# Performance work log

Measured on AMD Instinct MI355X. Metric: run time of the kernel, lower is better.

## Reference

```python
import jax, jax.numpy as jnp
import numpy as np

SEQ = 4096
E = 2048

def setup_inputs() -> dict:
    key = jax.random.key(0)
    kx, kq, kk, kv = jax.random.split(key, 4)
    scale = 1.0 / np.sqrt(E)
    x = jax.random.normal(kx, (SEQ, E), dtype=jnp.float32)
    # nn.Linear weights: shape [out, in], applied as x @ W.T
    Wq = jax.random.uniform(kq, (E, E), dtype=jnp.float32, minval=-scale, maxval=scale)
    Wk = jax.random.uniform(kk, (E, E), dtype=jnp.float32, minval=-scale, maxval=scale)
    Wv = jax.random.uniform(kv, (E, E), dtype=jnp.float32, minval=-scale, maxval=scale)
    return {"x": x, "Wq": Wq, "Wk": Wk, "Wv": Wv}

def reference(x, Wq, Wk, Wv):
    # q/k/v projections: nn.Linear(bias=False) -> x @ W.T
    q = x @ Wq.T  # [S, E]
    k = x @ Wk.T  # [S, E]
    v = x @ Wv.T  # [S, E]
    s = q @ k.T  # [S, S]
    w = jax.nn.softmax(s / jnp.sqrt(jnp.float32(E)), axis=-1)
    return w @ v  # [S, E]
```

## Files before the change

kernel.cpp:

```cpp
#include <hip/hip_runtime.h>
#include <hip/hip_bf16.h>

#define S_DIM 4096
#define E_DIM 2048

typedef __attribute__((ext_vector_type(4))) float f32x4;
typedef __attribute__((ext_vector_type(8))) short bf16x8;

__device__ __forceinline__ unsigned short f2bf(float f) {
  unsigned u = __builtin_bit_cast(unsigned, f);
  u += 0x7FFFu + ((u >> 16) & 1u);
  return (unsigned short)(u >> 16);
}
__device__ __forceinline__ float bf2f(unsigned short h) {
  return __builtin_bit_cast(float, ((unsigned)h) << 16);
}

__global__ __launch_bounds__(256) void cast_kernel(const float* __restrict__ in,
                                                   unsigned short* __restrict__ out,
                                                   int n4) {
  int i = blockIdx.x * 256 + threadIdx.x;
  if (i >= n4) return;
  float4 v = reinterpret_cast<const float4*>(in)[i];
  ushort4 o;
  o.x = f2bf(v.x); o.y = f2bf(v.y); o.z = f2bf(v.z); o.w = f2bf(v.w);
  reinterpret_cast<ushort4*>(out)[i] = o;
}

__global__ __launch_bounds__(256) void cast3_kernel(const float* __restrict__ w0,
                                                    const float* __restrict__ w1,
                                                    const float* __restrict__ w2,
                                                    unsigned short* __restrict__ out,
                                                    int n4each) {
  int i = blockIdx.x * 256 + threadIdx.x;
  if (i >= 3 * n4each) return;
  const float* src = (i < n4each) ? w0 : (i < 2 * n4each ? w1 : w2);
  int j = (i < n4each) ? i : (i < 2 * n4each ? i - n4each : i - 2 * n4each);
  float4 v = reinterpret_cast<const float4*>(src)[j];
  ushort4 o;
  o.x = f2bf(v.x); o.y = f2bf(v.y); o.z = f2bf(v.z); o.w = f2bf(v.w);
  reinterpret_cast<ushort4*>(out)[i] = o;
}

__device__ __forceinline__ void stage_half128(const unsigned short* __restrict__ g,
                                              int grow0, int ld, int kByte0,
                                              char* base, int tid) {
#pragma unroll
  for (int p = 0; p < 4; ++p) {
    const int o = (p * 256 + tid) * 16;
    const int S = o >> 10;
    const int oi = o & 1023;
    const int osi = oi ^ (((oi >> 9) & 1) << 5);
    const int r  = (S >> 1) * 16 + (osi >> 6);
    const int cb = (S & 1) * 64 + (osi & 63);
    const char* ga = reinterpret_cast<const char*>(g) +
                     ((size_t)(grow0 + r) * ld) * 2 + kByte0 + cb;
    char* la = base + (o & ~1023);
    __builtin_amdgcn_global_load_lds(
        (const __attribute__((address_space(1))) void*)ga,
        (__attribute__((address_space(3))) void*)la, 16, 0, 0);
  }
}


enum { EPI_QKV = 0, EPI_BF16 = 1, EPI_F32 = 2 };

template <int EPI>
__global__ __launch_bounds__(256, 2) void gemm128(
    const unsigned short* __restrict__ A, const unsigned short* __restrict__ B,
    int lda, int ldb, int K,
    float* __restrict__ Cf, unsigned short* __restrict__ Cb,
    unsigned short* __restrict__ Ct, int ldc, float scale) {
  extern __shared__ char lds[];

  const int tid = threadIdx.x;
  const int rowA0 = blockIdx.y * 128;
  const int rowB0 = blockIdx.x * 128;

  const int wave = tid >> 6;
  const int lane = tid & 63;
  const int wm = wave >> 1;
  const int wn = wave & 1;
  const int l15 = lane & 15;
  const int kg = lane >> 4;
  const int rsw = (l15 * 64 + kg * 16) ^ ((l15 & 8) << 2);
  const int aBase = wm * 8192;
  const int bBase = 16384 + wn * 8192;

  f32x4 acc[4][4];
#pragma unroll
  for (int mi = 0; mi < 4; ++mi)
#pragma unroll
    for (int ni = 0; ni < 4; ++ni) acc[mi][ni] = (f32x4){0.f, 0.f, 0.f, 0.f};

  const int NT = K / 64;
  char* buf0 = lds;
  char* buf1 = lds + 32768;

  stage_half128(A, rowA0, lda, 0,   buf0 + 0,     tid);
  stage_half128(B, rowB0, ldb, 0,   buf0 + 16384, tid);
  stage_half128(A, rowA0, lda, 128, buf1 + 0,     tid);
  stage_half128(B, rowB0, ldb, 128, buf1 + 16384, tid);
  asm volatile("s_waitcnt vmcnt(8)" ::: "memory");
  __builtin_amdgcn_sched_barrier(0);
  __builtin_amdgcn_s_barrier();

  for (int t = 0; t < NT; ++t) {
    char* bufc = lds + (t & 1) * 32768;
    bf16x8 af[4][2], bf[4][2];

#pragma unroll
    for (int mm = 0; mm < 4; ++mm)
#pragma unroll
      for (int ks = 0; ks < 2; ++ks)
        af[mm][ks] = *reinterpret_cast<const bf16x8*>(
            bufc + aBase + (mm * 2 + ks) * 1024 + rsw);
#pragma unroll
    for (int nn = 0; nn < 4; ++nn)
#pragma unroll
      for (int ks = 0; ks < 2; ++ks)
        bf[nn][ks] = *reinterpret_cast<const bf16x8*>(
            bufc + bBase + (nn * 2 + ks) * 1024 + rsw);
    __builtin_amdgcn_sched_barrier(0);
    __builtin_amdgcn_s_barrier();
    asm volatile("s_waitcnt lgkmcnt(0)" ::: "memory");
    __builtin_amdgcn_sched_barrier(0);
    __builtin_amdgcn_s_setprio(1);
#pragma unroll
    for (int mm = 0; mm < 4; ++mm)
#pragma unroll
      for (int nn = 0; nn < 4; ++nn)
        acc[mm][nn] = __builtin_amdgcn_mfma_f32_16x16x32_bf16(
            af[mm][0], bf[nn][0], acc[mm][nn], 0, 0, 0);
    __builtin_amdgcn_s_setprio(0);
    __builtin_amdgcn_s_barrier();

    if (t + 2 < NT) {
      const int kb = (t + 2) * 128;
      stage_half128(A, rowA0, lda, kb, bufc + 0,     tid);
      stage_half128(B, rowB0, ldb, kb, bufc + 16384, tid);
      asm volatile("s_waitcnt vmcnt(8)" ::: "memory");
    } else {
      asm volatile("s_waitcnt vmcnt(0)" ::: "memory");
    }
    __builtin_amdgcn_sched_barrier(0);
    __builtin_amdgcn_s_setprio(1);
#pragma unroll
    for (int mm = 0; mm < 4; ++mm)
#pragma unroll
      for (int nn = 0; nn < 4; ++nn)
        acc[mm][nn] = __builtin_amdgcn_mfma_f32_16x16x32_bf16(
            af[mm][1], bf[nn][1], acc[mm][nn], 0, 0, 0);
    __builtin_amdgcn_s_setprio(0);
    __builtin_amdgcn_sched_barrier(0);
    __builtin_amdgcn_s_barrier();
  }

  const int r0 = rowA0 + wm * 64;
  const int c0 = rowB0 + wn * 64;
#pragma unroll
  for (int mi = 0; mi < 4; ++mi) {
    const int row = r0 + mi * 16 + kg * 4;
#pragma unroll
    for (int ni = 0; ni < 4; ++ni) {
      const int col = c0 + ni * 16 + l15;
      f32x4 v = acc[mi][ni];
      if constexpr (EPI == EPI_F32) {
#pragma unroll
        for (int r = 0; r < 4; ++r)
          Cf[(size_t)(row + r) * ldc + col] = v[r];
      } else if constexpr (EPI == EPI_BF16) {
#pragma unroll
        for (int r = 0; r < 4; ++r)
          Cb[(size_t)(row + r) * ldc + col] = f2bf(v[r] * scale);
      } else {
        if (rowB0 < 4096) {
#pragma unroll
          for (int r = 0; r < 4; ++r)
            Cb[(size_t)(row + r) * 4096 + col] = f2bf(v[r]);
        } else {
          ushort4 pk;
          pk.x = f2bf(v[0]); pk.y = f2bf(v[1]);
          pk.z = f2bf(v[2]); pk.w = f2bf(v[3]);
          *reinterpret_cast<ushort4*>(Ct + (size_t)(col - 4096) * 4096 + row) = pk;
        }
      }
    }
  }
}

__global__ __launch_bounds__(256) void softmax_kernel(const unsigned short* __restrict__ Sm,
                                                      unsigned short* __restrict__ P) {
  const int row = blockIdx.x;
  const int tid = threadIdx.x;
  const unsigned short* src = Sm + (size_t)row * S_DIM;
  float vals[16];
  float mx = -1e30f;
#pragma unroll
  for (int i = 0; i < 4; ++i) {
    ushort4 h = reinterpret_cast<const ushort4*>(src)[tid + i * 256];
    float a = bf2f(h.x), b = bf2f(h.y), c = bf2f(h.z), d = bf2f(h.w);
    vals[i * 4 + 0] = a; vals[i * 4 + 1] = b;
    vals[i * 4 + 2] = c; vals[i * 4 + 3] = d;
    mx = fmaxf(mx, fmaxf(fmaxf(a, b), fmaxf(c, d)));
  }
#pragma unroll
  for (int off = 32; off >= 1; off >>= 1) mx = fmaxf(mx, __shfl_xor(mx, off, 64));
  __shared__ float red[8];
  const int wave = tid >> 6, lane = tid & 63;
  if (lane == 0) red[wave] = mx;
  __syncthreads();
  mx = fmaxf(fmaxf(red[0], red[1]), fmaxf(red[2], red[3]));
  float sum = 0.f;
#pragma unroll
  for (int i = 0; i < 16; ++i) { vals[i] = __expf(vals[i] - mx); sum += vals[i]; }
#pragma unroll
  for (int off = 32; off >= 1; off >>= 1) sum += __shfl_xor(sum, off, 64);
  if (lane == 0) red[4 + wave] = sum;
  __syncthreads();
  sum = red[4] + red[5] + red[6] + red[7];
  const float inv = 1.0f / sum;
  unsigned short* dst = P + (size_t)row * S_DIM;
#pragma unroll
  for (int i = 0; i < 4; ++i) {
    ushort4 pk;
    pk.x = f2bf(vals[i * 4 + 0] * inv);
    pk.y = f2bf(vals[i * 4 + 1] * inv);
    pk.z = f2bf(vals[i * 4 + 2] * inv);
    pk.w = f2bf(vals[i * 4 + 3] * inv);
    reinterpret_cast<ushort4*>(dst)[tid + i * 256] = pk;
  }
}

extern "C" void kernel_launch(void* const* d_in, const int* in_sizes, int n_in,
                              void* d_out, int out_size, void* d_ws, size_t ws_size,
                              hipStream_t stream) {
  const float* x  = (const float*)d_in[0];
  const float* Wq = (const float*)d_in[1];
  const float* Wk = (const float*)d_in[2];
  const float* Wv = (const float*)d_in[3];
  float* out = (float*)d_out;
  char* ws = (char*)d_ws;

  const size_t MB = 1024 * 1024;
  const size_t NEED = 120 * MB;
  if (ws_size < NEED) return;

  unsigned short* xb   = (unsigned short*)(ws);
  unsigned short* wcat = (unsigned short*)(ws + 16 * MB);
  unsigned short* qkb  = (unsigned short*)(ws + 40 * MB);
  unsigned short* vt   = (unsigned short*)(ws + 72 * MB);
  unsigned short* Sb   = (unsigned short*)(ws + 88 * MB);
  unsigned short* P = qkb;

  hipFuncSetAttribute(reinterpret_cast<const void*>(&gemm128<EPI_QKV>),
                      hipFuncAttributeMaxDynamicSharedMemorySize, 65536);
  hipFuncSetAttribute(reinterpret_cast<const void*>(&gemm128<EPI_BF16>),
                      hipFuncAttributeMaxDynamicSharedMemorySize, 65536);
  hipFuncSetAttribute(reinterpret_cast<const void*>(&gemm128<EPI_F32>),
                      hipFuncAttributeMaxDynamicSharedMemorySize, 65536);

  const int nx4 = S_DIM * E_DIM / 4;
  const int nw4 = E_DIM * E_DIM / 4;

  cast_kernel<<<nx4 / 256, 256, 0, stream>>>(x, xb, nx4);
  cast3_kernel<<<3 * nw4 / 256, 256, 0, stream>>>(Wq, Wk, Wv, wcat, nw4);

  gemm128<EPI_QKV><<<dim3(48, 32), 256, 65536, stream>>>(
      xb, wcat, E_DIM, E_DIM, E_DIM, nullptr, qkb, vt, 4096, 1.0f);

  const float scale = 0.022097086912079608f;
  gemm128<EPI_BF16><<<dim3(32, 32), 256, 65536, stream>>>(
      qkb, qkb + 2048, 4096, 4096, E_DIM, nullptr, Sb, nullptr, 4096, scale);

  softmax_kernel<<<S_DIM, 256, 0, stream>>>(Sb, P);

  gemm128<EPI_F32><<<dim3(16, 32), 256, 65536, stream>>>(
      P, vt, 4096, 4096, S_DIM, out, nullptr, nullptr, E_DIM, 1.0f);
}
```

Baseline: 400.0 us.

## Use 256x256 eight-wave ping-pong GEMM for the QK^T score computation

Adds a new 512-thread GEMM kernel with 256x256 output tiles, double-buffered 128KB LDS, and half-tile interleaving of global-to-LDS staging with MFMA compute using barriers and s_setprio. It replaces the 128x128 gemm128 launch for the S = QK^T product, raising arithmetic intensity per tile and overlapping loads with compute. The grid drops to 256 blocks and LDS use per block doubles, which may reduce occupancy and leave CUs underused on a large-CU device.

```diff
diff --git a/kernel.cpp b/kernel.cpp
--- a/kernel.cpp
+++ b/kernel.cpp
@@ -42,6 +42,26 @@
   reinterpret_cast<ushort4*>(out)[i] = o;
 }
 
+__device__ __forceinline__ void stage_half(const unsigned short* __restrict__ g,
+                                           int grow0, int ld, int kByte0,
+                                           char* ldsHalfBase, int tid) {
+#pragma unroll
+  for (int p = 0; p < 2; ++p) {
+    const int o = (p * 512 + tid) * 16;
+    const int S = o >> 10;
+    const int oi = o & 1023;
+    const int osi = oi ^ (((oi >> 9) & 1) << 5);
+    const int r  = (S >> 1) * 16 + (osi >> 6);
+    const int cb = (S & 1) * 64 + (osi & 63);
+    const char* ga = reinterpret_cast<const char*>(g) +
+                     ((size_t)(grow0 + r) * ld) * 2 + kByte0 + cb;
+    char* la = ldsHalfBase + (o & ~1023);
+    __builtin_amdgcn_global_load_lds(
+        (const __attribute__((address_space(1))) void*)ga,
+        (__attribute__((address_space(3))) void*)la, 16, 0, 0);
+  }
+}
+
 __device__ __forceinline__ void stage_half128(const unsigned short* __restrict__ g,
                                               int grow0, int ld, int kByte0,
                                               char* base, int tid) {
@@ -62,6 +82,140 @@
   }
 }
 
+#define MFMA_HALF(AM, AF)                                                      \
+  _Pragma("unroll") for (int ks = 0; ks < 2; ++ks)                             \
+  _Pragma("unroll") for (int mm = 0; mm < 4; ++mm) {                           \
+    acc[(AM) + mm][0] = __builtin_amdgcn_mfma_f32_16x16x32_bf16(               \
+        AF[mm][ks], b0[0][ks], acc[(AM) + mm][0], 0, 0, 0);                    \
+    acc[(AM) + mm][1] = __builtin_amdgcn_mfma_f32_16x16x32_bf16(               \
+        AF[mm][ks], b0[1][ks], acc[(AM) + mm][1], 0, 0, 0);                    \
+    acc[(AM) + mm][2] = __builtin_amdgcn_mfma_f32_16x16x32_bf16(               \
+        AF[mm][ks], b1[0][ks], acc[(AM) + mm][2], 0, 0, 0);                    \
+    acc[(AM) + mm][3] = __builtin_amdgcn_mfma_f32_16x16x32_bf16(               \
+        AF[mm][ks], b1[1][ks], acc[(AM) + mm][3], 0, 0, 0);                    \
+  }
+
+#define READ_A0Q(dst, buf)                                                     \
+  _Pragma("unroll") for (int mm = 0; mm < 4; ++mm)                             \
+  _Pragma("unroll") for (int ks = 0; ks < 2; ++ks)                             \
+    dst[mm][ks] = *reinterpret_cast<const bf16x8*>(                            \
+        (buf) + aBase + (mm * 2 + ks) * 1024 + rsw);
+
+#define READ_A1Q(dst, buf)                                                     \
+  _Pragma("unroll") for (int mm = 0; mm < 4; ++mm)                             \
+  _Pragma("unroll") for (int ks = 0; ks < 2; ++ks)                             \
+    dst[mm][ks] = *reinterpret_cast<const bf16x8*>(                            \
+        (buf) + aBase + ((4 + mm) * 2 + ks) * 1024 + rsw);
+
+#define READ_BQ(dst, buf, nh)                                                  \
+  _Pragma("unroll") for (int nn = 0; nn < 2; ++nn)                             \
+  _Pragma("unroll") for (int ks = 0; ks < 2; ++ks)                             \
+    dst[nn][ks] = *reinterpret_cast<const bf16x8*>(                            \
+        (buf) + bSub[nh][nn] + ks * 1024 + rsw);
+
+__global__ __launch_bounds__(512, 2) void gemm8(
+    const unsigned short* __restrict__ A, const unsigned short* __restrict__ B,
+    int lda, int ldb, int K,
+    unsigned short* __restrict__ Cb, int ldc, float scale) {
+  extern __shared__ char lds[];
+
+  const int tid = threadIdx.x;
+  const int rowA0 = blockIdx.y * 256;
+  const int rowB0 = blockIdx.x * 256;
+
+  const int wave = tid >> 6;
+  const int lane = tid & 63;
+  const int wm = wave >> 2;
+  const int wn = wave & 3;
+  const int l15 = lane & 15;
+  const int kg = lane >> 4;
+  const int rsw = (l15 * 64 + kg * 16) ^ ((l15 & 8) << 2);
+
+  int bSub[2][2];
+#pragma unroll
+  for (int nh = 0; nh < 2; ++nh)
+#pragma unroll
+    for (int nn = 0; nn < 2; ++nn) {
+      const int row = wn * 64 + nh * 32 + nn * 16;
+      bSub[nh][nn] = 32768 + (row >> 7) * 16384 + ((row & 127) >> 4) * 2048;
+    }
+  const int aBase = wm * 16384;
+
+  f32x4 acc[8][4];
+#pragma unroll
+  for (int mi = 0; mi < 8; ++mi)
+#pragma unroll
+    for (int ni = 0; ni < 4; ++ni) acc[mi][ni] = (f32x4){0.f, 0.f, 0.f, 0.f};
+
+  const int NT = K / 64;
+  char* buf0 = lds;
+  char* buf1 = lds + 65536;
+
+  stage_half(B, rowB0,       ldb, 0,   buf0 + 32768, tid);
+  stage_half(B, rowB0 + 128, ldb, 0,   buf0 + 49152, tid);
+  stage_half(A, rowA0,       lda, 0,   buf0 + 0,     tid);
+  stage_half(A, rowA0 + 128, lda, 0,   buf0 + 16384, tid);
+  stage_half(B, rowB0,       ldb, 128, buf1 + 32768, tid);
+  stage_half(B, rowB0 + 128, ldb, 128, buf1 + 49152, tid);
+  stage_half(A, rowA0,       lda, 128, buf1 + 0,     tid);
+  asm volatile("s_waitcnt vmcnt(6)" ::: "memory");
+  __builtin_amdgcn_sched_barrier(0);
+  __builtin_amdgcn_s_barrier();
+
+  for (int t = 0; t < NT; ++t) {
+    char* bufc = lds + (t & 1) * 65536;
+    char* bufn = lds + ((t & 1) ^ 1) * 65536;
+    bf16x8 a0[4][2], a1[4][2], b0[2][2], b1[2][2];
+
+    READ_A0Q(a0, bufc)
+    READ_BQ(b0, bufc, 0)
+    READ_BQ(b1, bufc, 1)
+    if (t + 1 < NT)
+      stage_half(A, rowA0 + 128, lda, (t + 1) * 128, bufn + 16384, tid);
+    __builtin_amdgcn_sched_barrier(0);
+    __builtin_amdgcn_s_barrier();
+    asm volatile("s_waitcnt lgkmcnt(0)" ::: "memory");
+    __builtin_amdgcn_sched_barrier(0);
+    __builtin_amdgcn_s_setprio(1);
+    MFMA_HALF(0, a0)
+    __builtin_amdgcn_s_setprio(0);
+    __builtin_amdgcn_s_barrier();
+
+    READ_A1Q(a1, bufc)
+    if (t + 2 < NT) {
+      const int kb = (t + 2) * 128;
+      stage_half(B, rowB0,       ldb, kb, bufc + 32768, tid);
+      stage_half(B, rowB0 + 128, ldb, kb, bufc + 49152, tid);
+      stage_half(A, rowA0,       lda, kb, bufc + 0,     tid);
+      asm volatile("s_waitcnt vmcnt(6)" ::: "memory");
+    } else {
+      asm volatile("s_waitcnt vmcnt(0)" ::: "memory");
+    }
+    __builtin_amdgcn_sched_barrier(0);
+    __builtin_amdgcn_s_barrier();
+    asm volatile("s_waitcnt lgkmcnt(0)" ::: "memory");
+    __builtin_amdgcn_sched_barrier(0);
+    __builtin_amdgcn_s_setprio(1);
+    MFMA_HALF(4, a1)
+    __builtin_amdgcn_s_setprio(0);
+    __builtin_amdgcn_s_barrier();
+  }
+
+  const int r0 = rowA0 + wm * 128;
+  const int c0 = rowB0 + wn * 64;
+#pragma unroll
+  for (int mi = 0; mi < 8; ++mi) {
+    const int row = r0 + (mi >> 2) * 64 + (mi & 3) * 16 + kg * 4;
+#pragma unroll
+    for (int ni = 0; ni < 4; ++ni) {
+      const int col = c0 + (ni >> 1) * 32 + (ni & 1) * 16 + l15;
+      f32x4 v = acc[mi][ni];
+#pragma unroll
+      for (int r = 0; r < 4; ++r)
+        Cb[(size_t)(row + r) * ldc + col] = f2bf(v[r] * scale);
+    }
+  }
+}
 
 enum { EPI_QKV = 0, EPI_BF16 = 1, EPI_F32 = 2 };
 
@@ -253,9 +407,9 @@
   unsigned short* Sb   = (unsigned short*)(ws + 88 * MB);
   unsigned short* P = qkb;
 
+  hipFuncSetAttribute(reinterpret_cast<const void*>(&gemm8),
+                      hipFuncAttributeMaxDynamicSharedMemorySize, 131072);
   hipFuncSetAttribute(reinterpret_cast<const void*>(&gemm128<EPI_QKV>),
-                      hipFuncAttributeMaxDynamicSharedMemorySize, 65536);
-  hipFuncSetAttribute(reinterpret_cast<const void*>(&gemm128<EPI_BF16>),
                       hipFuncAttributeMaxDynamicSharedMemorySize, 65536);
   hipFuncSetAttribute(reinterpret_cast<const void*>(&gemm128<EPI_F32>),
                       hipFuncAttributeMaxDynamicSharedMemorySize, 65536);
@@ -270,8 +424,8 @@
       xb, wcat, E_DIM, E_DIM, E_DIM, nullptr, qkb, vt, 4096, 1.0f);
 
   const float scale = 0.022097086912079608f;
-  gemm128<EPI_BF16><<<dim3(32, 32), 256, 65536, stream>>>(
-      qkb, qkb + 2048, 4096, 4096, E_DIM, nullptr, Sb, nullptr, 4096, scale);
+  gemm8<<<dim3(16, 16), 512, 131072, stream>>>(
+      qkb, qkb + 2048, 4096, 4096, E_DIM, Sb, 4096, scale);
 
   softmax_kernel<<<S_DIM, 256, 0, stream>>>(Sb, P);
 
```

Measured after the change: 373.7 us. -6.6%, faster.
